# Optimization experiments

Hardware: AMD Instinct MI355X
Metric: run time of the kernel (lower is better)

The kernel has to match this reference:

```python
import jax, jax.numpy as jnp
import numpy as np

B, P, N, H, W = 8, 4096, 1024, 1024, 1024


def setup_inputs() -> dict:
    key = jax.random.key(0)
    k1, k2, k3, k4 = jax.random.split(key, 4)
    return {
        "pred_points": jax.random.uniform(k1, (B, P, 2), dtype=jnp.float32),
        "dicts_coords": jax.random.uniform(k2, (B, N, 2), dtype=jnp.float32),
        "dicts_keys": jax.random.randint(k3, (B, N), 0, 1024, dtype=jnp.int64) if jax.config.jax_enable_x64 else jax.random.randint(k3, (B, N), 0, 1024).astype(jnp.int32),
        "masks": jax.random.randint(k4, (B, H, W), 0, 1025).astype(jnp.int32),
    }


def _match_single(U, V, keys, lm):
    # U: [P,2] normalized points, V: [N,2] gt coords, keys: [N] ids, lm: [H,W] label map
    h, w = lm.shape
    x = jnp.clip(jnp.round(U[:, 0] * h).astype(jnp.int32), 0, h - 1)
    y = jnp.clip(jnp.round(U[:, 1] * w).astype(jnp.int32), 0, w - 1)
    labels = lm[x, y]                                   # [P] label at each point
    # inside[j, p] == (mask for gt j covers point p); mask j is label channel keys[j]+1
    inside = labels[None, :] == (keys + 1)[:, None]     # [N,P] bool
    # full euclidean distance matrix gt->points
    D = jnp.sqrt(jnp.sum((V[:, None, :] - U[None, :, :]) ** 2, axis=-1))  # [N,P]
    inside_any = inside.any(axis=0)                     # points inside ANY mask
    avail0 = inside_any
    bg0 = ~inside_any                                   # background points
    idx = jnp.arange(U.shape[0])
    BIG = jnp.asarray(1e30, D.dtype)

    def step(carry, xs):
        avail, bg = carry
        ins_j, d_j = xs
        cand = ins_j & avail
        cnt = cand.sum()
        d_in = jnp.where(cand, d_j, BIG)
        u_in = jnp.argmin(d_in)                         # first-index tiebreak, like list order
        d_bg = jnp.where(bg, d_j, BIG)
        u_bg = jnp.argmin(d_bg)
        has_bg = bg.any()
        use_in = cnt > 0
        u = jnp.where(use_in, u_in, jnp.where(has_bg, u_bg, -1))
        cost = jnp.where(use_in, d_in[u_in], jnp.where(has_bg, d_bg[u_bg], jnp.asarray(0.0, D.dtype)))
        # inside-match consumes u from available; multi-point case dumps others into bg
        avail = jnp.where(use_in, avail & (idx != u_in), avail)
        others = cand & (idx != u_in)
        bg = jnp.where(use_in,
                       jnp.where(cnt > 1, bg | others, bg),
                       jnp.where(has_bg, bg & (idx != u_bg), bg))
        return (avail, bg), (u, cost)

    _, (src, costs) = jax.lax.scan(step, (avail0, bg0), (inside, D))
    tgt = jnp.where(src >= 0, jnp.arange(V.shape[0]), -1)
    return src, tgt, costs.sum()


def reference(pred_points, dicts_coords, dicts_keys, masks):
    # Returns padded matches per batch: src[b,j] = matched point index for gt j (-1 if skipped),
    # tgt[b,j] = j when matched else -1, total_cost[b] = sum of matched distances.
    src, tgt, total_cost = jax.vmap(_match_single)(pred_points, dicts_coords, dicts_keys, masks)
    return src, tgt, total_cost
```

## Files before the change

kernel.cpp:

```cpp
#include <hip/hip_runtime.h>
#include <stdint.h>

#define PPTS 4096
#define NGT  1024
#define HH   1024
#define WW   1024
#define EVPOOL_CAP 3072
#define BGCAP 160
#define RB 12

#define PART_BYTES (8 * 8 * 1025 * 2)
#define LAB_OFF    PART_BYTES
#define SPILL_OFF  (LAB_OFF + 8 * PPTS * 2)
#define SPILL_CAP  2048
#define WS_NEED    (SPILL_OFF + 8 * SPILL_CAP * 2)

typedef unsigned long long u64;

__device__ __forceinline__ float pdist2(float vx, float vy, float ux, float uy) {
    float dx = __fsub_rn(vx, ux);
    float dy = __fsub_rn(vy, uy);
    return __fadd_rn(__fmul_rn(dx, dx), __fmul_rn(dy, dy));
}

__global__ __launch_bounds__(512) void label_kernel(
    const float* __restrict__ pred, const int* __restrict__ masks,
    unsigned short* __restrict__ part, unsigned short* __restrict__ labs)
{
    __shared__ int lh[1025];
    const int blk = blockIdx.x, b = blk >> 3, sb = blk & 7;
    const int t = threadIdx.x;
    lh[t] = 0; lh[t + 512] = 0;
    if (t == 0) lh[1024] = 0;
    __syncthreads();
    const int p = (sb << 9) + t;
    float2 u = ((const float2*)(pred + (size_t)b * PPTS * 2))[p];
    int xi = (int)rintf(__fmul_rn(u.x, 1024.0f));
    int yi = (int)rintf(__fmul_rn(u.y, 1024.0f));
    xi = min(max(xi, 0), HH - 1);
    yi = min(max(yi, 0), WW - 1);
    int lab = (masks + (size_t)b * HH * WW)[xi * WW + yi];
    labs[(size_t)b * PPTS + p] = (unsigned short)lab;
    atomicAdd(&lh[lab], 1);
    __syncthreads();
    unsigned short* Pp = part + (size_t)b * 8200 + sb * 1025;
    Pp[t] = (unsigned short)lh[t];
    Pp[t + 512] = (unsigned short)lh[t + 512];
    if (t == 0) Pp[1024] = (unsigned short)lh[1024];
}

__global__ __launch_bounds__(1024) void matcher_kernel(
    const float* __restrict__ pred,
    const float* __restrict__ coords,
    const int*   __restrict__ keys,
    const int*   __restrict__ masks,
    float* __restrict__ out,
    const unsigned short* __restrict__ part, const unsigned short* __restrict__ labs,
    unsigned short* __restrict__ spill, int useWs, int B)
{
    __shared__ __align__(16) char regU[32768];
    __shared__ __align__(8)  char regE[8192];
    __shared__ __align__(8)  char regB[8200];
    __shared__ __align__(8)  char regP[2 * EVPOOL_CAP];
    __shared__ __align__(4)  char regS[384];
    __shared__ __align__(8)  char regT[2048];
    __shared__ u64            wScr64[16];
    __shared__ u64            sTot;
    __shared__ unsigned short evAx[1024];
    __shared__ unsigned short occList[NGT];
    __shared__ short          matchU[NGT];
    __shared__ unsigned       bgbits[PPTS / 32];
    __shared__ int            scal[4];
    __shared__ float2         vLds[NGT];
    __shared__ unsigned short gIdx[PPTS];
    __shared__ unsigned short gP[PPTS];
    __shared__ __align__(16) float2 gC[PPTS];

    float2*         bucketC  = (float2*)regU;
    unsigned short* ldsEnt   = (unsigned short*)regE;
    int*            bEnd     = (int*)regB;
    int*            occA     = ((int*)regB) + 1025;
    u64*            specWin  = (u64*)regB;
    unsigned*       cellCnt  = (unsigned*)(regB + 1280);
    int*            firstOcc = (int*)regP;
    unsigned short* evPool   = (unsigned short*)regP;
    unsigned*       present  = (unsigned*)regS;
    unsigned short* bgListSh = (unsigned short*)regS;
    unsigned short* bSt      = (unsigned short*)regT;
    float2*         vSteps   = (float2*)regT;
    int*   wScrI = (int*)wScr64;
    float* wScrF = (float*)wScr64;

    const int b = blockIdx.x;
    const int t = threadIdx.x;
    const int lane = t & 63, wv = t >> 6;
    const float* Ub = pred   + (size_t)b * PPTS * 2;
    const float2* Ub2 = (const float2*)Ub;
    const float* Vb = coords + (size_t)b * NGT * 2;
    const float2* Vb2 = (const float2*)Vb;
    const int*   Kb = keys   + (size_t)b * NGT;
    unsigned short* evSpillB = spill + (size_t)b * SPILL_CAP;
    const int spillCap = useWs ? SPILL_CAP : 0;

    if (t < PPTS / 32) bgbits[t] = 0;
    if (t == 0) scal[0] = 0;
    const int k1 = Kb[t] + 1;
    const float2 vMe = Vb2[t];
    vLds[t] = vMe;
    int lab[4]; float2 up[4];
    #pragma unroll
    for (int i = 0; i < 4; i++) up[i] = Ub2[t + (i << 10)];
    occA[t] = 0; firstOcc[t] = 0x7FFFFFFF;
    if (t == 0) { occA[1024] = 0; firstOcc[1024] = 0x7FFFFFFF; }
    if (t < 33) present[t] = 0;
    if (useWs) {
        const unsigned short* Pb = part + (size_t)b * 8200;
        int s = 0;
        #pragma unroll
        for (int sb = 0; sb < 8; sb++) s += Pb[sb * 1025 + t];
        bEnd[t] = s;
        if (t == 0) {
            int s2 = 0;
            #pragma unroll
            for (int sb = 0; sb < 8; sb++) s2 += Pb[sb * 1025 + 1024];
            bEnd[1024] = s2;
        }
        const unsigned short* Lb = labs + (size_t)b * PPTS;
        #pragma unroll
        for (int i = 0; i < 4; i++) lab[i] = Lb[t + (i << 10)];
    } else {
        bEnd[t] = 0;
        if (t == 0) bEnd[1024] = 0;
    }
    __syncthreads();
    atomicOr(&present[k1 >> 5], 1u << (k1 & 31));
    atomicAdd(&occA[k1], 1);
    atomicMin(&firstOcc[k1], t);
    if (!useWs) {
        const int* Mb = masks + (size_t)b * HH * WW;
        #pragma unroll
        for (int i = 0; i < 4; i++) {
            float2 u = up[i];
            int xi = (int)rintf(__fmul_rn(u.x, 1024.0f));
            int yi = (int)rintf(__fmul_rn(u.y, 1024.0f));
            xi = min(max(xi, 0), HH - 1);
            yi = min(max(yi, 0), WW - 1);
            lab[i] = Mb[xi * WW + yi];
            atomicAdd(&bEnd[lab[i]], 1);
        }
    }
    __syncthreads();

    {
        int c0 = bEnd[t], o0 = occA[t];
        bool pr0 = (present[t >> 5] >> (t & 31)) & 1u;
        int bCnt = bEnd[k1];
        int fo   = firstOcc[k1];
        int evc  = (fo == t && bCnt > 0) ? (bCnt - 1) : 0;
        u64 myv = (pr0 ? ((u64)(unsigned)c0 << 32) : ((u64)(unsigned)c0 << 48))
                  | ((u64)(unsigned)evc << 16) | (u64)(unsigned)o0;
        u64 add1 = 0; bool pr1 = false;
        if (t == 1023) {
            int c1 = bEnd[1024], o1 = occA[1024];
            pr1 = present[32] & 1u;
            add1 = (pr1 ? ((u64)(unsigned)c1 << 32) : ((u64)(unsigned)c1 << 48))
                   | (u64)(unsigned)o1;
        }
        u64 tot = myv + add1;
        u64 inc = tot;
        #pragma unroll
        for (int off = 1; off < 64; off <<= 1) {
            u64 n = __shfl_up(inc, off, 64);
            if (lane >= off) inc += n;
        }
        if (lane == 63) wScr64[wv] = inc;
        __syncthreads();
        if (t < 16) {
            u64 v = wScr64[t], inc2 = v;
            #pragma unroll
            for (int off = 1; off < 16; off <<= 1) {
                u64 n = __shfl_up(inc2, off, 64);
                if (t >= off) inc2 += n;
            }
            wScr64[t] = inc2 - v;
            if (t == 15) sTot = inc2;
        }
        __syncthreads();
        u64 excl = wScr64[wv] + inc - tot;
        int nBg0v = (int)(sTot >> 48);
        int bgS = (int)(excl >> 48);
        int prS = (int)((excl >> 32) & 0xFFFF);
        int evS = (int)((excl >> 16) & 0xFFFF);
        int ocS = (int)(excl & 0xFFFF);
        int start0 = pr0 ? (nBg0v + prS) : bgS;
        bEnd[t] = start0;
        occA[t] = ocS;
        evAx[t] = (unsigned short)evS;
        if (t >= 1) bSt[t - 1] = (unsigned short)start0;
        if (t == 1023) {
            u64 ex1 = excl + myv;
            int bgS1 = (int)(ex1 >> 48);
            int prS1 = (int)((ex1 >> 32) & 0xFFFF);
            int start1 = pr1 ? (nBg0v + prS1) : bgS1;
            bEnd[1024] = start1; occA[1024] = (int)(ex1 & 0xFFFF);
            bSt[1023] = (unsigned short)start1;
        }
    }
    __syncthreads();
    const int nBg0  = (int)(sTot >> 48);
    const int totEv = (int)((sTot >> 16) & 0xFFFF);
    const int EVcap = min(EVPOOL_CAP, PPTS - nBg0);

    #pragma unroll
    for (int i = 0; i < 4; i++) {
        int p = t + (i << 10);
        int slot = atomicAdd(&bEnd[lab[i]], 1);
        ldsEnt[slot] = (unsigned short)p;
        bucketC[slot] = up[i];
    }
    {
        int slot = atomicAdd(&occA[k1], 1);
        occList[slot] = (unsigned short)t;
    }
    __syncthreads();

    float costPartial = 0.0f;
    {
        const int l = t + 1;
        const int os = occA[t], oe = occA[l];
        for (int i = os + 1; i < oe; i++) {
            unsigned short v = occList[i];
            int k = i - 1;
            while (k >= os && occList[k] > v) { occList[k + 1] = occList[k]; k--; }
            occList[k + 1] = v;
        }
        const int bs = bSt[t], be = bEnd[l];
        const int bn = be - bs;
        if (oe > os && bn > 0 && bn <= RB) {
            float rcx[RB], rcy[RB]; int rp[RB];
            #pragma unroll
            for (int k = 0; k < RB; k++)
                if (k < bn) { float2 c = bucketC[bs + k]; rcx[k] = c.x; rcy[k] = c.y;
                              rp[k] = ldsEnt[bs + k]; }
            unsigned cons = 0;
            for (int o = os; o < oe; o++) {
                int j = occList[o];
                float2 v = vLds[j];
                u64 best = ~0ull;
                #pragma unroll
                for (int k = 0; k < RB; k++) {
                    if (k < bn && !((cons >> k) & 1u)) {
                        float d2 = pdist2(v.x, v.y, rcx[k], rcy[k]);
                        u64 pk = ((u64)__float_as_uint(d2) << 24)
                                 | ((u64)(unsigned)rp[k] << 12) | (u64)(unsigned)k;
                        if (pk < best) best = pk;
                    }
                }
                if (best != ~0ull) {
                    int eW = (int)(best & 0xFFFull);
                    matchU[j] = (short)((best >> 12) & 0xFFFull);
                    costPartial = __fadd_rn(costPartial,
                        __fsqrt_rn(__uint_as_float((unsigned)(best >> 24))));
                    cons |= 1u << eW;
                    if (o == os) {
                        int base = evAx[j];
                        #pragma unroll
                        for (int k = 0; k < RB; k++) {
                            if (k < bn && k != eW) {
                                int idx = base + k - (k > eW ? 1 : 0);
                                if (idx < EVcap) evPool[idx] = (unsigned short)(bs + k);
                                else if (idx - EVcap < spillCap)
                                    evSpillB[idx - EVcap] = (unsigned short)rp[k];
                            }
                        }
                    }
                } else matchU[j] = -2;
            }
        } else if (oe > os) {
            u64 cons = 0;
            for (int o = os; o < oe; o++) {
                int j = occList[o];
                float2 v = vLds[j];
                u64 best = ~0ull;
                int avail = 0;
                for (int e = bs; e < be; e++) {
                    int eIdx = e - bs;
                    int p = ldsEnt[e];
                    bool consd;
                    if (eIdx < 64) consd = (cons >> eIdx) & 1ull;
                    else {
                        consd = false;
                        for (int o2 = os; o2 < o; o2++)
                            if ((int)matchU[occList[o2]] == p) { consd = true; break; }
                    }
                    if (consd) continue;
                    avail++;
                    float2 u = bucketC[e];
                    float d2 = pdist2(v.x, v.y, u.x, u.y);
                    u64 pk = ((u64)__float_as_uint(d2) << 24) | ((u64)(unsigned)p << 12)
                             | (u64)(unsigned)eIdx;
                    if (pk < best) best = pk;
                }
                if (avail > 0) {
                    int eW = (int)(best & 0xFFFull);
                    matchU[j] = (short)((best >> 12) & 0xFFFull);
                    costPartial = __fadd_rn(costPartial,
                        __fsqrt_rn(__uint_as_float((unsigned)(best >> 24))));
                    if (eW < 64) cons |= 1ull << eW;
                    if (o == os) {
                        int base = evAx[j], w3 = 0;
                        for (int e = bs; e < be; e++) {
                            if (e - bs == eW) continue;
                            int idx = base + w3;
                            if (idx < EVcap) evPool[idx] = (unsigned short)e;
                            else if (idx - EVcap < spillCap)
                                evSpillB[idx - EVcap] = ldsEnt[e];
                            w3++;
                        }
                    }
                } else matchU[j] = -2;
            }
        }
    }
    __syncthreads();

    {
        bool need = (matchU[t] == (short)-2);
        u64 m = __ballot(need);
        if (lane == 0) wScrI[wv] = __popcll(m);
    }
    __syncthreads();
    if (t < 64) {
        int orig = (t < 16) ? wScrI[t] : 0;
        int v = orig;
        #pragma unroll
        for (int off = 1; off <= 8; off <<= 1) {
            int n = __shfl_up(v, off, 64);
            if (t >= off) v += n;
        }
        if (t < 16) wScrI[t] = v - orig;
        if (t == 15) scal[0] = v;
    }
    __syncthreads();
    {
        bool need = (matchU[t] == (short)-2);
        u64 m = __ballot(need);
        if (need) {
            int rank = __popcll(m & ((1ull << lane) - 1ull));
            int idx = wScrI[wv] + rank;
            if (idx < BGCAP) { bgListSh[idx] = (unsigned short)t; vSteps[idx] = vMe; }
        }
    }
    __syncthreads();

    const int bgCnt = min(scal[0], BGCAP);
    {
        const int nStage = min(totEv, EVcap);
        float2 sc[4]; unsigned short sp[4];
        #pragma unroll
        for (int k = 0; k < 4; k++) {
            int i = t + (k << 10);
            if (i < nStage) { int slot = evPool[i]; sp[k] = ldsEnt[slot]; sc[k] = bucketC[slot]; }
        }
        __syncthreads();
        #pragma unroll
        for (int k = 0; k < 4; k++) {
            int i = t + (k << 10);
            if (i < nStage) { ldsEnt[nBg0 + i] = sp[k]; bucketC[nBg0 + i] = sc[k]; }
        }
    }
    __syncthreads();

    if (bgCnt > 0) {
        const int nT = nBg0 + min(totEv, EVcap);
        cellCnt[t] = 0;
        __syncthreads();
        int myCell[4];
        #pragma unroll
        for (int k = 0; k < 4; k++) {
            int i = t + (k << 10);
            myCell[k] = -1;
            if (i < nT) {
                float2 c = bucketC[i];
                int cx = min(31, max(0, (int)__fmul_rn(c.x, 32.0f)));
                int cy = min(31, max(0, (int)__fmul_rn(c.y, 32.0f)));
                myCell[k] = (cx << 5) | cy;
                atomicAdd(&cellCnt[myCell[k]], 1);
            }
        }
        __syncthreads();
        {
            unsigned c0 = cellCnt[t];
            unsigned inc = c0;
            #pragma unroll
            for (int off = 1; off < 64; off <<= 1) {
                unsigned n = __shfl_up(inc, off, 64);
                if (lane >= off) inc += n;
            }
            if (lane == 63) wScrI[wv] = (int)inc;
            __syncthreads();
            if (t < 16) {
                int v = wScrI[t], inc2 = v;
                #pragma unroll
                for (int off = 1; off < 16; off <<= 1) {
                    int n = __shfl_up(inc2, off, 64);
                    if (t >= off) inc2 += n;
                }
                wScrI[t] = inc2 - v;
            }
            __syncthreads();
            unsigned excl = (unsigned)wScrI[wv] + inc - c0;
            cellCnt[t] = excl;
            __syncthreads();
        }
        #pragma unroll
        for (int k = 0; k < 4; k++) {
            if (myCell[k] >= 0) {
                int i = t + (k << 10);
                int slot = atomicAdd(&cellCnt[myCell[k]], 1);
                gIdx[slot] = (unsigned short)i;
                gP[slot]   = ldsEnt[i];
                gC[slot]   = bucketC[i];
            }
        }
        __syncthreads();
        for (int s = wv; s < bgCnt; s += 16) {
            const int js = bgListSh[s];
            const float2 v = vSteps[s];
            const int lim = nBg0 + min((int)evAx[js], EVcap);
            const int cx = min(31, max(0, (int)__fmul_rn(v.x, 32.0f)));
            const int cy = min(31, max(0, (int)__fmul_rn(v.y, 32.0f)));
            u64 best = ~0ull;
            for (int r = 0; r <= 31; r++) {
                if (r >= 1) {
                    float gap = __fmul_rn((float)(r - 1), 0.03125f) - 1e-6f;
                    if (gap > 0.0f) {
                        float bd2 = __uint_as_float((unsigned)(best >> 32));
                        if (bd2 < __fmul_rn(gap, gap)) break;
                    }
                }
                const int ncells = (r == 0) ? 1 : 8 * r;
                for (int ci = lane; ci < ncells; ci += 64) {
                    int dx, dy;
                    if (r == 0) { dx = 0; dy = 0; }
                    else if (ci < 2 * r)      { dx = -r + ci;            dy = -r; }
                    else if (ci < 4 * r)      { dx = r;                  dy = -r + (ci - 2 * r); }
                    else if (ci < 6 * r)      { dx = r - (ci - 4 * r);   dy = r; }
                    else                      { dx = -r;                 dy = r - (ci - 6 * r); }
                    int x = cx + dx, y = cy + dy;
                    if ((unsigned)x < 32u && (unsigned)y < 32u) {
                        int c = (x << 5) | y;
                        int beg = c ? (int)cellCnt[c - 1] : 0;
                        int end = (int)cellCnt[c];
                        for (int i2 = beg; i2 < end; i2++) {
                            if (gIdx[i2] < lim) {
                                float2 cc = gC[i2];
                                float d2 = pdist2(v.x, v.y, cc.x, cc.y);
                                u64 pk = ((u64)__float_as_uint(d2) << 32) | gP[i2];
                                if (pk < best) best = pk;
                            }
                        }
                    }
                }
                #pragma unroll
                for (int off = 32; off >= 1; off >>= 1) {
                    u64 o = __shfl_xor(best, off, 64);
                    if (o < best) best = o;
                }
            }
            const int ne = evAx[js];
            if (ne > EVcap && spillCap > 0) {
                for (int ei = EVcap + lane; ei < ne; ei += 64) {
                    if (ei - EVcap >= spillCap) break;
                    unsigned p = evSpillB[ei - EVcap];
                    float2 c = Ub2[p];
                    float d2 = pdist2(v.x, v.y, c.x, c.y);
                    u64 pk = ((u64)__float_as_uint(d2) << 32) | p;
                    if (pk < best) best = pk;
                }
                #pragma unroll
                for (int off = 32; off >= 1; off >>= 1) {
                    u64 o = __shfl_xor(best, off, 64);
                    if (o < best) best = o;
                }
            }
            if (lane == 0) specWin[s] = best;
        }
    }
    __syncthreads();

    {
        int done = 0;
        for (;;) {
            if (t == 0) scal[3] = bgCnt;
            __syncthreads();
            if (t >= done && t < bgCnt) {
                u64 w = specWin[t];
                if (w != ~0ull) {
                    unsigned p = (unsigned)(w & 0xFFFFFFFFull);
                    bool inval = (bgbits[p >> 5] >> (p & 31)) & 1u;
                    if (!inval) {
                        for (int s2 = done; s2 < t; s2++) {
                            u64 w2 = specWin[s2];
                            if (w2 != ~0ull &&
                                (unsigned)(w2 & 0xFFFFFFFFull) == p) { inval = true; break; }
                        }
                    }
                    if (inval) atomicMin(&scal[3], t);
                }
            }
            __syncthreads();
            const int fs = scal[3];
            if (fs >= bgCnt) break;
            if (t >= done && t < fs) {
                u64 w = specWin[t];
                if (w != ~0ull) {
                    unsigned p = (unsigned)(w & 0xFFFFFFFFull);
                    atomicOr(&bgbits[p >> 5], 1u << (p & 31));
                }
            }
            __syncthreads();
            {
                const int js = bgListSh[fs];
                const float2 v = vSteps[fs];
                const int ne = evAx[js];
                const int lim = nBg0 + min(ne, EVcap);
                u64 best = ~0ull;
                for (int i = t; i < lim; i += 1024) {
                    unsigned p = ldsEnt[i];
                    if (!((bgbits[p >> 5] >> (p & 31)) & 1u)) {
                        float2 c = bucketC[i];
                        float d2 = pdist2(v.x, v.y, c.x, c.y);
                        u64 pk = ((u64)__float_as_uint(d2) << 32) | p;
                        if (pk < best) best = pk;
                    }
                }
                for (int ei = EVcap + t; ei < ne; ei += 1024) {
                    if (ei - EVcap >= spillCap) break;
                    unsigned p = evSpillB[ei - EVcap];
                    if (!((bgbits[p >> 5] >> (p & 31)) & 1u)) {
                        float2 c = Ub2[p];
                        float d2 = pdist2(v.x, v.y, c.x, c.y);
                        u64 pk = ((u64)__float_as_uint(d2) << 32) | p;
                        if (pk < best) best = pk;
                    }
                }
                #pragma unroll
                for (int off = 32; off >= 1; off >>= 1) {
                    u64 o = __shfl_xor(best, off, 64);
                    if (o < best) best = o;
                }
                if (lane == 0) wScr64[wv] = best;
                __syncthreads();
                if (t == 0) {
                    u64 bb = wScr64[0];
                    for (int i = 1; i < 16; i++) if (wScr64[i] < bb) bb = wScr64[i];
                    specWin[fs] = bb;
                    if (bb != ~0ull) {
                        unsigned p = (unsigned)(bb & 0xFFFFFFFFull);
                        bgbits[p >> 5] |= 1u << (p & 31);
                    }
                }
            }
            done = fs + 1;
        }
    }
    if (t < bgCnt) {
        const int js = bgListSh[t];
        u64 w0 = specWin[t];
        if (w0 == ~0ull) matchU[js] = -1;
        else {
            matchU[js] = (short)(w0 & 0xFFFFFFFFull);
            costPartial = __fadd_rn(costPartial,
                __fsqrt_rn(__uint_as_float((unsigned)(w0 >> 32))));
        }
    }
    __syncthreads();

    {
        float cp = costPartial;
        #pragma unroll
        for (int off = 32; off >= 1; off >>= 1) cp += __shfl_xor(cp, off, 64);
        if (lane == 0) wScrF[wv] = cp;
    }
    __syncthreads();
    if (t == 0) {
        float tot = 0.0f;
        for (int i = 0; i < 16; ++i) tot = __fadd_rn(tot, wScrF[i]);
        out[(size_t)2 * B * NGT + b] = tot;
    }
    {
        int u = matchU[t];
        out[(size_t)b * NGT + t] = (float)u;
        out[(size_t)B * NGT + (size_t)b * NGT + t] = (u >= 0) ? (float)t : -1.0f;
    }
}

extern "C" void kernel_launch(void* const* d_in, const int* in_sizes, int n_in,
                              void* d_out, int out_size, void* d_ws, size_t ws_size,
                              hipStream_t stream) {
    const float* pred   = (const float*)d_in[0];
    const float* coords = (const float*)d_in[1];
    const int*   keys   = (const int*)d_in[2];
    const int*   masks  = (const int*)d_in[3];
    float* out = (float*)d_out;
    int B = in_sizes[2] / NGT;
    int useWs = (B == 8 && ws_size >= (size_t)WS_NEED) ? 1 : 0;
    unsigned short* partP  = (unsigned short*)d_ws;
    unsigned short* labsP  = (unsigned short*)((char*)d_ws + LAB_OFF);
    unsigned short* spillP = (unsigned short*)((char*)d_ws + SPILL_OFF);
    if (useWs) {
        label_kernel<<<B * 8, 512, 0, stream>>>(pred, masks, partP, labsP);
    }
    matcher_kernel<<<B, 1024, 0, stream>>>(pred, coords, keys, masks, out,
                                           partP, labsP, spillP, useWs, B);
}
```

Baseline: 114.3 us.

## Transpose partial histograms, fold cell binning into bucketing, batch first grid rings

The prep kernel now writes per-subblock label histograms transposed, so the matcher sums them with one 16-byte vector load per thread instead of eight strided loads. Grid-cell assignment and counting for the background nearest-neighbour search move into the existing bucketing and staging loops, with cell ids kept in a new LDS array. This removes a separate pass and its barriers but adds LDS usage and extra atomics even when no background steps occur. The ring search now scans the 5x5 neighbourhood in one parallel pass per wavefront, does a wave min-reduction, then continues from ring 3, cutting per-ring loop overhead for typical queries.

```diff
diff --git a/kernel.cpp b/kernel.cpp
--- a/kernel.cpp
+++ b/kernel.cpp
@@ -43,10 +43,10 @@
     labs[(size_t)b * PPTS + p] = (unsigned short)lab;
     atomicAdd(&lh[lab], 1);
     __syncthreads();
-    unsigned short* Pp = part + (size_t)b * 8200 + sb * 1025;
-    Pp[t] = (unsigned short)lh[t];
-    Pp[t + 512] = (unsigned short)lh[t + 512];
-    if (t == 0) Pp[1024] = (unsigned short)lh[1024];
+    unsigned short* Pp = part + (size_t)b * 8200;
+    Pp[t * 8 + sb] = (unsigned short)lh[t];
+    Pp[(t + 512) * 8 + sb] = (unsigned short)lh[t + 512];
+    if (t == 0) Pp[1024 * 8 + sb] = (unsigned short)lh[1024];
 }
 
 __global__ __launch_bounds__(1024) void matcher_kernel(
@@ -72,6 +72,8 @@
     __shared__ unsigned       bgbits[PPTS / 32];
     __shared__ int            scal[4];
     __shared__ float2         vLds[NGT];
+    __shared__ unsigned       cellCnt[1024];
+    __shared__ unsigned short cellOf[PPTS];
     __shared__ unsigned short gIdx[PPTS];
     __shared__ unsigned short gP[PPTS];
     __shared__ __align__(16) float2 gC[PPTS];
@@ -81,7 +83,6 @@
     int*            bEnd     = (int*)regB;
     int*            occA     = ((int*)regB) + 1025;
     u64*            specWin  = (u64*)regB;
-    unsigned*       cellCnt  = (unsigned*)(regB + 1280);
     int*            firstOcc = (int*)regP;
     unsigned short* evPool   = (unsigned short*)regP;
     unsigned*       present  = (unsigned*)regS;
@@ -104,6 +105,7 @@
 
     if (t < PPTS / 32) bgbits[t] = 0;
     if (t == 0) scal[0] = 0;
+    cellCnt[t] = 0;
     const int k1 = Kb[t] + 1;
     const float2 vMe = Vb2[t];
     vLds[t] = vMe;
@@ -115,15 +117,18 @@
     if (t < 33) present[t] = 0;
     if (useWs) {
         const unsigned short* Pb = part + (size_t)b * 8200;
-        int s = 0;
-        #pragma unroll
-        for (int sb = 0; sb < 8; sb++) s += Pb[sb * 1025 + t];
+        const uint4 pv = reinterpret_cast<const uint4*>(Pb)[t];
+        int s = (int)(pv.x & 0xFFFFu) + (int)(pv.x >> 16)
+              + (int)(pv.y & 0xFFFFu) + (int)(pv.y >> 16)
+              + (int)(pv.z & 0xFFFFu) + (int)(pv.z >> 16)
+              + (int)(pv.w & 0xFFFFu) + (int)(pv.w >> 16);
         bEnd[t] = s;
         if (t == 0) {
-            int s2 = 0;
-            #pragma unroll
-            for (int sb = 0; sb < 8; sb++) s2 += Pb[sb * 1025 + 1024];
-            bEnd[1024] = s2;
+            const uint4 p1 = reinterpret_cast<const uint4*>(Pb)[1024];
+            bEnd[1024] = (int)(p1.x & 0xFFFFu) + (int)(p1.x >> 16)
+                       + (int)(p1.y & 0xFFFFu) + (int)(p1.y >> 16)
+                       + (int)(p1.z & 0xFFFFu) + (int)(p1.z >> 16)
+                       + (int)(p1.w & 0xFFFFu) + (int)(p1.w >> 16);
         }
         const unsigned short* Lb = labs + (size_t)b * PPTS;
         #pragma unroll
@@ -217,6 +222,13 @@
         int slot = atomicAdd(&bEnd[lab[i]], 1);
         ldsEnt[slot] = (unsigned short)p;
         bucketC[slot] = up[i];
+        if (!((present[lab[i] >> 5] >> (lab[i] & 31)) & 1u)) {
+            int cx = min(31, max(0, (int)__fmul_rn(up[i].x, 32.0f)));
+            int cy = min(31, max(0, (int)__fmul_rn(up[i].y, 32.0f)));
+            int cell = (cx << 5) | cy;
+            cellOf[slot] = (unsigned short)cell;
+            atomicAdd(&cellCnt[cell], 1u);
+        }
     }
     {
         int slot = atomicAdd(&occA[k1], 1);
@@ -366,29 +378,20 @@
         #pragma unroll
         for (int k = 0; k < 4; k++) {
             int i = t + (k << 10);
-            if (i < nStage) { ldsEnt[nBg0 + i] = sp[k]; bucketC[nBg0 + i] = sc[k]; }
+            if (i < nStage) {
+                ldsEnt[nBg0 + i] = sp[k]; bucketC[nBg0 + i] = sc[k];
+                int cx = min(31, max(0, (int)__fmul_rn(sc[k].x, 32.0f)));
+                int cy = min(31, max(0, (int)__fmul_rn(sc[k].y, 32.0f)));
+                int cell = (cx << 5) | cy;
+                cellOf[nBg0 + i] = (unsigned short)cell;
+                atomicAdd(&cellCnt[cell], 1u);
+            }
         }
     }
     __syncthreads();
 
     if (bgCnt > 0) {
         const int nT = nBg0 + min(totEv, EVcap);
-        cellCnt[t] = 0;
-        __syncthreads();
-        int myCell[4];
-        #pragma unroll
-        for (int k = 0; k < 4; k++) {
-            int i = t + (k << 10);
-            myCell[k] = -1;
-            if (i < nT) {
-                float2 c = bucketC[i];
-                int cx = min(31, max(0, (int)__fmul_rn(c.x, 32.0f)));
-                int cy = min(31, max(0, (int)__fmul_rn(c.y, 32.0f)));
-                myCell[k] = (cx << 5) | cy;
-                atomicAdd(&cellCnt[myCell[k]], 1);
-            }
-        }
-        __syncthreads();
         {
             unsigned c0 = cellCnt[t];
             unsigned inc = c0;
@@ -415,9 +418,10 @@
         }
         #pragma unroll
         for (int k = 0; k < 4; k++) {
-            if (myCell[k] >= 0) {
-                int i = t + (k << 10);
-                int slot = atomicAdd(&cellCnt[myCell[k]], 1);
+            int i = t + (k << 10);
+            if (i < nT) {
+                int cell = cellOf[i];
+                int slot = (int)atomicAdd(&cellCnt[cell], 1u);
                 gIdx[slot] = (unsigned short)i;
                 gP[slot]   = ldsEnt[i];
                 gC[slot]   = bucketC[i];
@@ -431,19 +435,35 @@
             const int cx = min(31, max(0, (int)__fmul_rn(v.x, 32.0f)));
             const int cy = min(31, max(0, (int)__fmul_rn(v.y, 32.0f)));
             u64 best = ~0ull;
-            for (int r = 0; r <= 31; r++) {
-                if (r >= 1) {
-                    float gap = __fmul_rn((float)(r - 1), 0.03125f) - 1e-6f;
-                    if (gap > 0.0f) {
-                        float bd2 = __uint_as_float((unsigned)(best >> 32));
-                        if (bd2 < __fmul_rn(gap, gap)) break;
-                    }
-                }
-                const int ncells = (r == 0) ? 1 : 8 * r;
+            if (lane < 25) {
+                int x = cx + (lane / 5) - 2, y = cy + (lane % 5) - 2;
+                if ((unsigned)x < 32u && (unsigned)y < 32u) {
+                    int c = (x << 5) | y;
+                    int beg = c ? (int)cellCnt[c - 1] : 0;
+                    int end = (int)cellCnt[c];
+                    for (int i2 = beg; i2 < end; i2++) {
+                        if (gIdx[i2] < lim) {
+                            float2 cc = gC[i2];
+                            float d2 = pdist2(v.x, v.y, cc.x, cc.y);
+                            u64 pk = ((u64)__float_as_uint(d2) << 32) | gP[i2];
+                            if (pk < best) best = pk;
+                        }
+                    }
+                }
+            }
+            #pragma unroll
+            for (int off = 32; off >= 1; off >>= 1) {
+                u64 o = __shfl_xor(best, off, 64);
+                if (o < best) best = o;
+            }
+            for (int r = 3; r <= 31; r++) {
+                float gap = __fmul_rn((float)(r - 1), 0.03125f) - 1e-6f;
+                float bd2 = __uint_as_float((unsigned)(best >> 32));
+                if (bd2 < __fmul_rn(gap, gap)) break;
+                const int ncells = 8 * r;
                 for (int ci = lane; ci < ncells; ci += 64) {
                     int dx, dy;
-                    if (r == 0) { dx = 0; dy = 0; }
-                    else if (ci < 2 * r)      { dx = -r + ci;            dy = -r; }
+                    if (ci < 2 * r)           { dx = -r + ci;            dy = -r; }
                     else if (ci < 4 * r)      { dx = r;                  dy = -r + (ci - 2 * r); }
                     else if (ci < 6 * r)      { dx = r - (ci - 4 * r);   dy = r; }
                     else                      { dx = -r;                 dy = r - (ci - 6 * r); }
```

Result: faster. 110.3 us (-3.5%).
